# Kernel optimization log

Hardware: AMD Instinct MI355X
Metric: run time of the kernel (lower is better)

The kernel has to match this reference:

```python
import jax, jax.numpy as jnp
import numpy as np

B, DIM, IN_DIM, H, W = 4, 512, 256, 64, 64
DOWN = IN_DIM // 2          # 128
QK = DOWN // 8              # 16
EPS = 1e-5


def conv2d(x, w, b, pad=0, dil=1):
    y = jax.lax.conv_general_dilated(
        x, w, window_strides=(1, 1),
        padding=[(pad, pad), (pad, pad)],
        rhs_dilation=(dil, dil),
        dimension_numbers=('NCHW', 'OIHW', 'NCHW'))
    return y + b[None, :, None, None]


def bn(x, g, bt, m, v):
    # inference-mode BatchNorm2d with running stats
    scale = (g * jax.lax.rsqrt(v + EPS))[None, :, None, None]
    return (x - m[None, :, None, None]) * scale + bt[None, :, None, None]


def prelu(x, a):
    return jnp.where(x >= 0, x, a * x)


def setup_inputs() -> dict:
    key = jax.random.key(0)
    ks = iter(jax.random.split(key, 64))
    d = {}
    d['x'] = jax.random.normal(next(ks), (B, DIM, H, W), dtype=jnp.float32)

    def conv_params(name, cout, cin, k):
        d[name + '_w'] = jax.random.normal(next(ks), (cout, cin, k, k), jnp.float32) * 0.05
        d[name + '_b'] = jax.random.normal(next(ks), (cout,), jnp.float32) * 0.05

    def bn_params(name, c):
        d[name + '_g'] = 1.0 + 0.1 * jax.random.normal(next(ks), (c,), jnp.float32)
        d[name + '_bt'] = 0.1 * jax.random.normal(next(ks), (c,), jnp.float32)
        d[name + '_m'] = 0.1 * jax.random.normal(next(ks), (c,), jnp.float32)
        d[name + '_v'] = 0.5 + jax.random.uniform(next(ks), (c,), jnp.float32)

    def prelu_param(name):
        d[name] = jnp.full((1,), 0.25, jnp.float32)

    conv_params('dc', IN_DIM, DIM, 3);  bn_params('dc_bn', IN_DIM); prelu_param('dc_a')
    conv_params('c1', DOWN, IN_DIM, 1); bn_params('c1_bn', DOWN);   prelu_param('c1_a')
    conv_params('c2', DOWN, IN_DIM, 3); bn_params('c2_bn', DOWN);   prelu_param('c2_a')
    conv_params('q', QK, DOWN, 1)
    conv_params('k', QK, DOWN, 1)
    conv_params('v', DOWN, DOWN, 1)
    d['gamma2'] = jnp.full((1,), 0.1, jnp.float32)  # torch init is 0; nonzero to exercise the path
    conv_params('c3', DOWN, IN_DIM, 1); bn_params('c3_bn', DOWN);   prelu_param('c3_a')
    conv_params('f', IN_DIM, 3 * DOWN, 1); bn_params('f_bn', IN_DIM); prelu_param('f_a')
    return d


def reference(x,
              dc_w, dc_b, dc_bn_g, dc_bn_bt, dc_bn_m, dc_bn_v, dc_a,
              c1_w, c1_b, c1_bn_g, c1_bn_bt, c1_bn_m, c1_bn_v, c1_a,
              c2_w, c2_b, c2_bn_g, c2_bn_bt, c2_bn_m, c2_bn_v, c2_a,
              q_w, q_b, k_w, k_b, v_w, v_b, gamma2,
              c3_w, c3_b, c3_bn_g, c3_bn_bt, c3_bn_m, c3_bn_v, c3_a,
              f_w, f_b, f_bn_g, f_bn_bt, f_bn_m, f_bn_v, f_a):
    # down_conv: 3x3 conv + BN + PReLU
    x = prelu(bn(conv2d(x, dc_w, dc_b, pad=1), dc_bn_g, dc_bn_bt, dc_bn_m, dc_bn_v), dc_a)
    # branch 1: 1x1 conv
    c1 = prelu(bn(conv2d(x, c1_w, c1_b), c1_bn_g, c1_bn_bt, c1_bn_m, c1_bn_v), c1_a)
    # branch 2: dilated 3x3 conv + non-local self-attention
    c2 = prelu(bn(conv2d(x, c2_w, c2_b, pad=2, dil=2), c2_bn_g, c2_bn_bt, c2_bn_m, c2_bn_v), c2_a)
    b, c, h, w = c2.shape
    hw = h * w
    q = conv2d(c2, q_w, q_b).reshape(b, QK, hw)   # [B, C/8, HW]
    k = conv2d(c2, k_w, k_b).reshape(b, QK, hw)
    v = conv2d(c2, v_w, v_b).reshape(b, c, hw)
    energy = jnp.einsum('bcn,bcm->bnm', q, k)     # [B, HW, HW]
    attn = jax.nn.softmax(energy, axis=-1)
    out2 = jnp.einsum('bcm,bnm->bcn', v, attn).reshape(b, c, h, w)
    out2 = gamma2 * out2 + c2
    # branch 3: global avg pool -> 1x1 conv -> broadcast (bilinear upsample of 1x1 is constant)
    pooled = jnp.mean(x, axis=(2, 3), keepdims=True)  # [B, IN_DIM, 1, 1]
    c3 = prelu(bn(conv2d(pooled, c3_w, c3_b), c3_bn_g, c3_bn_bt, c3_bn_m, c3_bn_v), c3_a)
    c3 = jnp.broadcast_to(c3, (b, DOWN, h, w))
    # fuse
    cat = jnp.concatenate([c1, out2, c3], axis=1)
    return prelu(bn(conv2d(cat, f_w, f_b), f_bn_g, f_bn_bt, f_bn_m, f_bn_v), f_a)
```

## Files before the change

### kernel.cpp

```cpp
#include <hip/hip_runtime.h>
#include <hip/hip_bf16.h>
#include <math.h>

#define HW 4096
#define EPSV 1e-5f

typedef unsigned short ushort;
typedef __attribute__((ext_vector_type(8))) short bf16x8;
typedef __attribute__((ext_vector_type(4))) float f32x4;

__device__ inline ushort f2bf(float f) {
    __hip_bfloat16 h = __float2bfloat16(f);
    return *reinterpret_cast<ushort*>(&h);
}
__device__ inline float bf2f(ushort u) {
    unsigned int v = ((unsigned int)u) << 16;
    return __uint_as_float(v);
}

template<int C>
__global__ __launch_bounds__(256) void to_chlast_bf16(
    const float* __restrict__ src, ushort* __restrict__ dst)
{
    const int b = blockIdx.z, c0 = blockIdx.y * 64, p0 = blockIdx.x * 64;
    const int tid = threadIdx.x;
    __shared__ float sT[64][65];
    for (int i = tid; i < 4096; i += 256) {
        const int ch = i >> 6, px = i & 63;
        sT[ch][px] = src[(size_t)(b * C + c0 + ch) * HW + p0 + px];
    }
    __syncthreads();
    const int px = tid >> 2, seg = tid & 3;
    ushort tmp[16];
    #pragma unroll
    for (int j = 0; j < 16; ++j) tmp[j] = f2bf(sT[seg * 16 + j][px]);
    ushort* d = dst + (size_t)(b * HW + p0 + px) * C + c0 + seg * 16;
    *(uint4*)d = *(uint4*)&tmp[0];
    *(uint4*)(d + 8) = *(uint4*)&tmp[8];
}

template<int CIN, int COUT>
__global__ __launch_bounds__(256) void pack_w3x3(
    const float* __restrict__ w, ushort* __restrict__ wpk)
{
    const int idx = blockIdx.x * 256 + threadIdx.x;
    constexpr int total = 9 * (CIN / 32) * COUT * 32;
    if (idx >= total) return;
    const int ci_in = idx & 31;
    int rest = idx >> 5;
    const int co = rest % COUT; rest /= COUT;
    const int cc = rest % (CIN / 32);
    const int tap = rest / (CIN / 32);
    wpk[idx] = f2bf(w[((size_t)co * CIN + cc * 32 + ci_in) * 9 + tap]);
}

__global__ __launch_bounds__(256) void pack_w1x1(
    const float* __restrict__ w, ushort* __restrict__ o,
    int K, int stride, int total)
{
    const int idx = blockIdx.x * 256 + threadIdx.x;
    if (idx >= total) return;
    const int co = idx / K, k = idx - co * K;
    o[idx] = f2bf(w[(size_t)co * stride + k]);
}

__global__ __launch_bounds__(256) void zero_pool(float* __restrict__ p)
{
    p[blockIdx.x * 256 + threadIdx.x] = 0.f;
}

template<int CIN, int COUT, int COTILE, int DIL, int ROWS, int OMODE>
__global__ __launch_bounds__(256, OMODE == 0 ? 4 : 2) void conv3x3_fused(
    const ushort* __restrict__ xin,
    const ushort* __restrict__ wpk,
    const float* __restrict__ bias, const float* __restrict__ bng,
    const float* __restrict__ bnb, const float* __restrict__ bnm,
    const float* __restrict__ bnv, const float* __restrict__ al,
    void* __restrict__ outv,
    float* __restrict__ pool)
{
    constexpr int HR = ROWS + 2 * DIL;
    constexpr int NC = 64 + 2 * DIL;
    constexpr int MT = COTILE / 16;
    constexpr int WPR = 4 / ROWS;
    constexpr int NT = ROWS;
    constexpr int SAS = 40;
    constexpr int CH = CIN / 32;
    constexpr int NA = HR * NC * 4;
    constexpr int NREG = (NA + 255) / 256;
    constexpr int WCH = 9 * MT * 64;
    constexpr int WPT = (WCH + 255) / 256;

    const int tid = threadIdx.x;
    const int wave = tid >> 6, lane = tid & 63;
    const int l15 = lane & 15, quad = lane >> 4;
    const int b = blockIdx.z;
    const int cob = blockIdx.y;
    const int co0 = cob * COTILE;
    const int h0 = blockIdx.x * ROWS;
    const int row = wave / WPR;
    const int ntbase = (wave % WPR) * NT;

    __shared__ __align__(16) ushort sA[HR * NC * SAS];
    __shared__ __align__(16) ushort sW[WCH * 8];

    f32x4 acc[MT][NT];
    #pragma unroll
    for (int mt = 0; mt < MT; ++mt)
        #pragma unroll
        for (int nt = 0; nt < NT; ++nt) acc[mt][nt] = (f32x4){0.f, 0.f, 0.f, 0.f};

    #pragma unroll 1
    for (int cc = 0; cc < CH; ++cc) {
        if (cc != 0) __syncthreads();
        #pragma unroll
        for (int k = 0; k < NREG; ++k) {
            const int i = tid + k * 256;
            if (i < NA) {
                const int p = i >> 2, seg = i & 3;
                const int r = p / NC, c = p - r * NC;
                const int grow = h0 - DIL + r, gcol = c - DIL;
                uint4 val = {0u, 0u, 0u, 0u};
                if (grow >= 0 && grow < 64 && gcol >= 0 && gcol < 64)
                    val = *(const uint4*)&xin[((size_t)(b * 64 + grow) * 64 + gcol) * CIN
                                              + cc * 32 + seg * 8];
                *(uint4*)&sA[p * SAS + seg * 8] = val;
            }
        }
        #pragma unroll
        for (int k = 0; k < WPT; ++k) {
            const int i = tid + k * 256;
            if (i < WCH) {
                const int tap = i / (MT * 64);
                const int r = i - tap * (MT * 64);
                const int mt = r >> 6, n = r & 63;
                const uint4 wv = *(const uint4*)&wpk[
                    ((size_t)(tap * (CIN / 32) + cc) * COUT + co0 + mt * 16 + (n & 15)) * 32
                    + (n >> 4) * 8];
                *(uint4*)&sW[i * 8] = wv;
            }
        }
        __syncthreads();

        #pragma unroll
        for (int tap = 0; tap < 9; ++tap) {
            const int ty = tap / 3, tx = tap - ty * 3;
            const int rl = row + ty * DIL;
            bf16x8 wf[MT];
            #pragma unroll
            for (int mt = 0; mt < MT; ++mt)
                wf[mt] = *(const bf16x8*)&sW[((tap * MT + mt) * 64 + lane) * 8];
            #pragma unroll
            for (int nt = 0; nt < NT; ++nt) {
                const int cl = (ntbase + nt) * 16 + l15 + tx * DIL;
                const bf16x8 bp = *(const bf16x8*)&sA[(rl * NC + cl) * SAS + quad * 8];
                #pragma unroll
                for (int mt = 0; mt < MT; ++mt)
                    acc[mt][nt] = __builtin_amdgcn_mfma_f32_16x16x32_bf16(
                        wf[mt], bp, acc[mt][nt], 0, 0, 0);
            }
        }
    }

    const float a = al[0];

    if constexpr (OMODE == 0) {
        __syncthreads();
        ushort* sT = sA;
        #pragma unroll
        for (int mt = 0; mt < MT; ++mt) {
            float sc[4], sh[4], psum[4];
            #pragma unroll
            for (int rr = 0; rr < 4; ++rr) {
                const int co = co0 + mt * 16 + quad * 4 + rr;
                sc[rr] = bng[co] * rsqrtf(bnv[co] + EPSV);
                sh[rr] = (bias[co] - bnm[co]) * sc[rr] + bnb[co];
                psum[rr] = 0.f;
            }
            #pragma unroll
            for (int nt = 0; nt < NT; ++nt) {
                float tv[4];
                #pragma unroll
                for (int rr = 0; rr < 4; ++rr) {
                    float t = acc[mt][nt][rr] * sc[rr] + sh[rr];
                    t = t >= 0.f ? t : a * t;
                    tv[rr] = t;
                    psum[rr] += t;
                }
                ushort4 u;
                u.x = f2bf(tv[0]); u.y = f2bf(tv[1]);
                u.z = f2bf(tv[2]); u.w = f2bf(tv[3]);
                const int px = (ntbase + nt) * 16 + l15;
                *(ushort4*)&sT[(row * 64 + px) * 40 + mt * 16 + quad * 4] = u;
            }
            #pragma unroll
            for (int rr = 0; rr < 4; ++rr) {
                float v = psum[rr];
                v += __shfl_xor(v, 1);
                v += __shfl_xor(v, 2);
                v += __shfl_xor(v, 4);
                v += __shfl_xor(v, 8);
                if (l15 == 0)
                    atomicAdd(&pool[b * 256 + co0 + mt * 16 + quad * 4 + rr], v);
            }
        }
        __syncthreads();
        ushort* dst = (ushort*)outv;
        const int p = tid >> 1, half = tid & 1;
        const uint4 v0 = *(const uint4*)&sT[p * 40 + half * 16];
        const uint4 v1 = *(const uint4*)&sT[p * 40 + half * 16 + 8];
        const size_t off = ((size_t)(b * 4096 + (h0 + (p >> 6)) * 64 + (p & 63))) * 256
                           + co0 + half * 16;
        *(uint4*)&dst[off] = v0;
        *(uint4*)&dst[off + 8] = v1;
    } else {
        float* out = (float*)outv;
        #pragma unroll
        for (int mt = 0; mt < MT; ++mt)
            #pragma unroll
            for (int rr = 0; rr < 4; ++rr) {
                const int co = co0 + mt * 16 + quad * 4 + rr;
                const float sc = bng[co] * rsqrtf(bnv[co] + EPSV);
                const float sh = (bias[co] - bnm[co]) * sc + bnb[co];
                #pragma unroll
                for (int nt = 0; nt < NT; ++nt) {
                    float t = acc[mt][nt][rr] * sc + sh;
                    t = t >= 0.f ? t : a * t;
                    out[((size_t)(b * COUT + co) * 64 + h0 + row) * 64
                        + (ntbase + nt) * 16 + l15] = t;
                }
            }
    }
}

template<int CIN, int COUT, bool BNACT, int OMODE>
__global__ __launch_bounds__(256) void gemm1x1_cl(
    const ushort* __restrict__ xin,
    const ushort* __restrict__ wbf,
    const float* __restrict__ bias, const float* __restrict__ bng,
    const float* __restrict__ bnb, const float* __restrict__ bnm,
    const float* __restrict__ bnv, const float* __restrict__ al,
    const float* __restrict__ ebias, void* __restrict__ outv,
    int ostride, int ocol)
{
    const int tid = threadIdx.x;
    const int wave = tid >> 6, lane = tid & 63;
    const int l15 = lane & 15, quad = lane >> 4;
    const int pix0 = blockIdx.x * 128 + wave * 32;
    const int co0 = blockIdx.y * 64;

    f32x4 acc[4][2];
    #pragma unroll
    for (int mt = 0; mt < 4; ++mt)
        #pragma unroll
        for (int nt = 0; nt < 2; ++nt) acc[mt][nt] = (f32x4){0.f, 0.f, 0.f, 0.f};

    #pragma unroll 2
    for (int cc = 0; cc < CIN / 32; ++cc) {
        bf16x8 aw[4], bp[2];
        #pragma unroll
        for (int mt = 0; mt < 4; ++mt)
            aw[mt] = *(const bf16x8*)&wbf[(size_t)(co0 + mt * 16 + l15) * CIN + cc * 32 + quad * 8];
        #pragma unroll
        for (int nt = 0; nt < 2; ++nt)
            bp[nt] = *(const bf16x8*)&xin[(size_t)(pix0 + nt * 16 + l15) * CIN + cc * 32 + quad * 8];
        #pragma unroll
        for (int mt = 0; mt < 4; ++mt)
            #pragma unroll
            for (int nt = 0; nt < 2; ++nt)
                acc[mt][nt] = __builtin_amdgcn_mfma_f32_16x16x32_bf16(
                    aw[mt], bp[nt], acc[mt][nt], 0, 0, 0);
    }

    const int bI = pix0 >> 12;
    const float a = BNACT ? al[0] : 0.f;

    if (OMODE == 0) {
        float* out = (float*)outv;
        #pragma unroll
        for (int mt = 0; mt < 4; ++mt)
            #pragma unroll
            for (int r = 0; r < 4; ++r) {
                const int co = co0 + mt * 16 + quad * 4 + r;
                float bb = bias[co];
                if (ebias) bb += ebias[bI * COUT + co];
                float scale = 1.f, shift = bb;
                if (BNACT) {
                    scale = bng[co] * rsqrtf(bnv[co] + EPSV);
                    shift = bb * scale + (bnb[co] - bnm[co] * scale);
                }
                #pragma unroll
                for (int nt = 0; nt < 2; ++nt) {
                    float t = acc[mt][nt][r] * scale + shift;
                    if (BNACT) t = t >= 0.f ? t : a * t;
                    out[((size_t)(bI * COUT + co)) * HW + (pix0 & 4095) + nt * 16 + l15] = t;
                }
            }
    } else {
        __shared__ ushort sT[4][32][68];
        #pragma unroll
        for (int mt = 0; mt < 4; ++mt)
            #pragma unroll
            for (int r = 0; r < 4; ++r) {
                const int co = co0 + mt * 16 + quad * 4 + r;
                float bb = bias[co];
                float scale = 1.f, shift = bb;
                if (BNACT) {
                    scale = bng[co] * rsqrtf(bnv[co] + EPSV);
                    shift = bb * scale + (bnb[co] - bnm[co] * scale);
                }
                #pragma unroll
                for (int nt = 0; nt < 2; ++nt) {
                    float t = acc[mt][nt][r] * scale + shift;
                    if (BNACT) t = t >= 0.f ? t : a * t;
                    sT[wave][nt * 16 + l15][mt * 16 + quad * 4 + r] = f2bf(t);
                }
            }
        __syncthreads();
        const int p = lane >> 1, half = lane & 1;
        ushort* out = (ushort*)outv;
        #pragma unroll
        for (int seg = 0; seg < 4; ++seg) {
            uint2 a0 = *(uint2*)&sT[wave][p][half * 32 + seg * 8];
            uint2 a1 = *(uint2*)&sT[wave][p][half * 32 + seg * 8 + 4];
            uint4 vv = {a0.x, a0.y, a1.x, a1.y};
            *(uint4*)&out[(size_t)(pix0 + p) * ostride + ocol + co0 + half * 32 + seg * 8] = vv;
        }
    }
}

template<int CIN, bool BNACT, bool OUTBF16>
__global__ __launch_bounds__(256) void conv1x1_kernel(
    const float* __restrict__ in0,
    const float* __restrict__ wgt, int wstride, int COUT,
    const float* __restrict__ bias, const float* __restrict__ al,
    void* __restrict__ outv)
{
    const int tid = threadIdx.x;
    const int b = blockIdx.z, co0 = blockIdx.y * 64, p0 = blockIdx.x * 64;
    const int cg = tid >> 4, pg = tid & 15;
    const int c0l = cg * 4, w0 = pg * 4;

    __shared__ __align__(16) float sIn[16 * 64];
    __shared__ __align__(16) float sW[16 * 68];

    float acc[4][4] = {};

    for (int cc = 0; cc < CIN; cc += 16) {
        {
            int i = tid;
            #pragma unroll
            for (int it = 0; it < 4; ++it, i += 256) {
                const int px = i & 63, ci = i >> 6;
                sIn[ci * 64 + px] = in0[(size_t)(b * CIN + cc + ci) * HW + p0 + px];
            }
            i = tid;
            #pragma unroll
            for (int it = 0; it < 4; ++it, i += 256) {
                const int ci = i & 15, co = i >> 4;
                sW[ci * 68 + co] = wgt[(co0 + co) * wstride + cc + ci];
            }
        }
        __syncthreads();
        #pragma unroll
        for (int ci = 0; ci < 16; ++ci) {
            const float4 iv = *(const float4*)&sIn[ci * 64 + w0];
            const float4 wv = *(const float4*)&sW[ci * 68 + c0l];
            const float ia[4] = {iv.x, iv.y, iv.z, iv.w};
            const float wa[4] = {wv.x, wv.y, wv.z, wv.w};
            #pragma unroll
            for (int i2 = 0; i2 < 4; ++i2)
                #pragma unroll
                for (int j = 0; j < 4; ++j)
                    acc[i2][j] = fmaf(wa[i2], ia[j], acc[i2][j]);
        }
        __syncthreads();
    }

    const float a = BNACT ? al[0] : 0.f;
    #pragma unroll
    for (int i2 = 0; i2 < 4; ++i2) {
        const int co = co0 + c0l + i2;
        const float shift = bias[co];
        float r[4];
        #pragma unroll
        for (int j = 0; j < 4; ++j) {
            float t = acc[i2][j] + shift;
            r[j] = (BNACT && t < 0.f) ? a * t : t;
        }
        const size_t base = (size_t)(b * COUT + co) * HW + p0 + w0;
        if (OUTBF16) {
            ushort* out = (ushort*)outv;
            #pragma unroll
            for (int j = 0; j < 4; ++j) out[base + j] = f2bf(r[j]);
        } else {
            float* out = (float*)outv;
            *(float4*)&out[base] = make_float4(r[0], r[1], r[2], r[3]);
        }
    }
}

__global__ __launch_bounds__(256) void qk_kernel(
    const float* __restrict__ c2g, const float* __restrict__ qw,
    const float* __restrict__ qb2, const float* __restrict__ kw,
    const float* __restrict__ kb2, ushort* __restrict__ qpack,
    ushort* __restrict__ kpack)
{
    const int b = blockIdx.y, p0 = blockIdx.x * 64, tid = threadIdx.x;
    __shared__ float sC[128][64];
    __shared__ float sWq[16][128];
    __shared__ float sWk[16][128];
    for (int i = tid; i < 8192; i += 256) {
        const int px = i & 63, ci = i >> 6;
        sC[ci][px] = c2g[(size_t)(b * 128 + ci) * HW + p0 + px];
    }
    for (int i = tid; i < 2048; i += 256) {
        const int ci = i & 127, co = i >> 7;
        sWq[co][ci] = qw[co * 128 + ci];
        sWk[co][ci] = kw[co * 128 + ci];
    }
    __syncthreads();
    const int px = tid & 63, grp = tid >> 6;
    const int co0 = (grp & 1) * 8;
    const bool isK = grp >= 2;
    const float* sWp = isK ? &sWk[0][0] : &sWq[0][0];
    float acc[8] = {};
    for (int ci = 0; ci < 128; ++ci) {
        const float xv = sC[ci][px];
        #pragma unroll
        for (int j = 0; j < 8; ++j)
            acc[j] = fmaf(sWp[(co0 + j) * 128 + ci], xv, acc[j]);
    }
    const float* bsrc = isK ? kb2 : qb2;
    ushort* osrc = isK ? kpack : qpack;
    const size_t base = (size_t)(b * 4096 + p0 + px) * 32;
    #pragma unroll
    for (int j = 0; j < 8; ++j) {
        osrc[base + co0 + j] = f2bf(acc[j] + bsrc[co0 + j]);
        osrc[base + 16 + co0 + j] = 0;
    }
}

__global__ __launch_bounds__(256) void attn_flash(
    const ushort* __restrict__ qpack,
    const ushort* __restrict__ kpack,
    const ushort* __restrict__ vpackT,
    ushort* __restrict__ opart,
    float* __restrict__ Mpart,
    float* __restrict__ Spart)
{
    const int tid = threadIdx.x;
    const int wave = tid >> 6, lane = tid & 63;
    const int l15 = lane & 15, quad = lane >> 4;
    const int b = blockIdx.z, j = blockIdx.y;
    const int n0w = blockIdx.x * 128 + wave * 32;
    const int m_begin = j * 512;

    __shared__ __align__(16) ushort sV[2][128][40];
    __shared__ __align__(16) ushort sP[4][2][16][40];

    const bf16x8 bq0 = *(const bf16x8*)(qpack + ((size_t)(b * 4096 + n0w + l15) * 32 + quad * 8));
    const bf16x8 bq1 = *(const bf16x8*)(qpack + ((size_t)(b * 4096 + n0w + 16 + l15) * 32 + quad * 8));
    const f32x4 z = {0.f, 0.f, 0.f, 0.f};

    float runM0 = -3e30f, runM1 = -3e30f;
    #pragma unroll 2
    for (int t = 0; t < 8; ++t) {
        const int m0 = m_begin + t * 64;
        #pragma unroll
        for (int ms = 0; ms < 4; ++ms) {
            const bf16x8 ak = *(const bf16x8*)(
                kpack + ((size_t)(b * 4096 + m0 + ms * 16 + l15) * 32 + quad * 8));
            const f32x4 s0 = __builtin_amdgcn_mfma_f32_16x16x32_bf16(ak, bq0, z, 0, 0, 0);
            const f32x4 s1 = __builtin_amdgcn_mfma_f32_16x16x32_bf16(ak, bq1, z, 0, 0, 0);
            runM0 = fmaxf(runM0, fmaxf(fmaxf(s0[0], s0[1]), fmaxf(s0[2], s0[3])));
            runM1 = fmaxf(runM1, fmaxf(fmaxf(s1[0], s1[1]), fmaxf(s1[2], s1[3])));
        }
    }
    runM0 = fmaxf(runM0, __shfl_xor(runM0, 16));
    runM0 = fmaxf(runM0, __shfl_xor(runM0, 32));
    runM1 = fmaxf(runM1, __shfl_xor(runM1, 16));
    runM1 = fmaxf(runM1, __shfl_xor(runM1, 32));
    const float Ms0 = runM0 * 1.44269504f;
    const float Ms1 = runM1 * 1.44269504f;

    float runS0 = 0.f, runS1 = 0.f;
    f32x4 oacc0[8], oacc1[8];
    #pragma unroll
    for (int cs = 0; cs < 8; ++cs) {
        oacc0[cs] = (f32x4){0.f, 0.f, 0.f, 0.f};
        oacc1[cs] = (f32x4){0.f, 0.f, 0.f, 0.f};
    }

    const int stc = tid >> 1, stseg = tid & 1;

    {
        uint4 v0 = *(const uint4*)&vpackT[(size_t)(b * 128 + stc) * HW + m_begin + stseg * 16];
        uint4 v1 = *(const uint4*)&vpackT[(size_t)(b * 128 + stc) * HW + m_begin + stseg * 16 + 8];
        *(uint4*)&sV[0][stc][stseg * 16] = v0;
        *(uint4*)&sV[0][stc][stseg * 16 + 8] = v1;
    }
    __syncthreads();

    #pragma unroll 1
    for (int t = 0; t < 16; ++t) {
        const int m0 = m_begin + t * 32;
        const int buf = t & 1;
        uint4 nv0, nv1;
        const bool more = (t + 1 < 16);
        if (more) {
            const size_t nb = (size_t)(b * 128 + stc) * HW + m0 + 32 + stseg * 16;
            nv0 = *(const uint4*)&vpackT[nb];
            nv1 = *(const uint4*)&vpackT[nb + 8];
        }
        f32x4 s0[2], s1[2];
        #pragma unroll
        for (int ms = 0; ms < 2; ++ms) {
            const bf16x8 ak = *(const bf16x8*)(
                kpack + ((size_t)(b * 4096 + m0 + ms * 16 + l15) * 32 + quad * 8));
            s0[ms] = __builtin_amdgcn_mfma_f32_16x16x32_bf16(ak, bq0, z, 0, 0, 0);
            s1[ms] = __builtin_amdgcn_mfma_f32_16x16x32_bf16(ak, bq1, z, 0, 0, 0);
        }
        #pragma unroll
        for (int ms = 0; ms < 2; ++ms) {
            float p0[4], p1[4];
            #pragma unroll
            for (int r = 0; r < 4; ++r) {
                p0[r] = __builtin_amdgcn_exp2f(fmaf(s0[ms][r], 1.44269504f, -Ms0));
                p1[r] = __builtin_amdgcn_exp2f(fmaf(s1[ms][r], 1.44269504f, -Ms1));
                runS0 += p0[r];
                runS1 += p1[r];
            }
            ushort4 u0, u1;
            u0.x = f2bf(p0[0]); u0.y = f2bf(p0[1]); u0.z = f2bf(p0[2]); u0.w = f2bf(p0[3]);
            u1.x = f2bf(p1[0]); u1.y = f2bf(p1[1]); u1.z = f2bf(p1[2]); u1.w = f2bf(p1[3]);
            *(uint2*)&sP[wave][0][l15][ms * 16 + quad * 4] = *(uint2*)&u0;
            *(uint2*)&sP[wave][1][l15][ms * 16 + quad * 4] = *(uint2*)&u1;
        }
        asm volatile("s_waitcnt lgkmcnt(0)" ::: "memory");
        const bf16x8 ap0 = *(const bf16x8*)&sP[wave][0][l15][quad * 8];
        const bf16x8 ap1 = *(const bf16x8*)&sP[wave][1][l15][quad * 8];
        #pragma unroll
        for (int cs = 0; cs < 8; ++cs) {
            const bf16x8 bv = *(const bf16x8*)&sV[buf][cs * 16 + l15][quad * 8];
            oacc0[cs] = __builtin_amdgcn_mfma_f32_16x16x32_bf16(ap0, bv, oacc0[cs], 0, 0, 0);
            oacc1[cs] = __builtin_amdgcn_mfma_f32_16x16x32_bf16(ap1, bv, oacc1[cs], 0, 0, 0);
        }
        if (more) {
            *(uint4*)&sV[buf ^ 1][stc][stseg * 16] = nv0;
            *(uint4*)&sV[buf ^ 1][stc][stseg * 16 + 8] = nv1;
            __syncthreads();
        }
    }

    runS0 += __shfl_xor(runS0, 16);
    runS0 += __shfl_xor(runS0, 32);
    runS1 += __shfl_xor(runS1, 16);
    runS1 += __shfl_xor(runS1, 32);
    if (lane < 32) {
        const float Mv = (lane < 16) ? runM0 : runM1;
        const float Sv = (lane < 16) ? runS0 : runS1;
        const int n = n0w + ((lane < 16) ? 0 : 16) + l15;
        Mpart[((size_t)b * 8 + j) * 4096 + n] = Mv;
        Spart[((size_t)b * 8 + j) * 4096 + n] = Sv;
    }
    #pragma unroll
    for (int cs = 0; cs < 8; ++cs)
        #pragma unroll
        for (int r = 0; r < 4; ++r) {
            const int n = n0w + quad * 4 + r;
            opart[(((size_t)b * 8 + j) * 4096 + n) * 128 + cs * 16 + l15] = f2bf(oacc0[cs][r]);
            opart[(((size_t)b * 8 + j) * 4096 + n + 16) * 128 + cs * 16 + l15] = f2bf(oacc1[cs][r]);
        }
}

__global__ __launch_bounds__(256) void attn_combine(
    const ushort* __restrict__ opart, const float* __restrict__ Mpart,
    const float* __restrict__ Spart, const float* __restrict__ c2g,
    const float* __restrict__ gamma2, ushort* __restrict__ catb)
{
    const int b = blockIdx.y, n0 = blockIdx.x * 32, tid = threadIdx.x;
    __shared__ float sC2[128][33];
    __shared__ float sWj[8][32];
    if (tid < 32) {
        const int n = n0 + tid;
        float Mj[8], Sj[8];
        #pragma unroll
        for (int j = 0; j < 8; ++j) {
            Mj[j] = Mpart[((size_t)b * 8 + j) * 4096 + n];
            Sj[j] = Spart[((size_t)b * 8 + j) * 4096 + n];
        }
        float M = -3e30f;
        #pragma unroll
        for (int j = 0; j < 8; ++j) M = fmaxf(M, Mj[j]);
        float St = 0.f, e[8];
        #pragma unroll
        for (int j = 0; j < 8; ++j) { e[j] = __expf(Mj[j] - M); St += Sj[j] * e[j]; }
        const float inv = 1.0f / St;
        #pragma unroll
        for (int j = 0; j < 8; ++j) sWj[j][tid] = e[j] * inv;
    }
    #pragma unroll
    for (int e = 0; e < 16; ++e) {
        const int idx = tid + e * 256;
        const int c = idx >> 5, n = idx & 31;
        sC2[c][n] = c2g[(size_t)(b * 128 + c) * HW + n0 + n];
    }
    __syncthreads();
    const float g2 = gamma2[0];
    #pragma unroll
    for (int e = 0; e < 16; ++e) {
        const int idx = tid + e * 256;
        const int n = idx >> 7, c = idx & 127;
        float s = 0.f;
        #pragma unroll
        for (int j = 0; j < 8; ++j)
            s += bf2f(opart[(((size_t)b * 8 + j) * 4096 + n0 + n) * 128 + c]) * sWj[j][n];
        catb[(size_t)(b * 4096 + n0 + n) * 256 + 128 + c] = f2bf(fmaf(g2, s, sC2[c][n]));
    }
}

__global__ __launch_bounds__(256) void c3_fbias_kernel(
    const float* __restrict__ pool, const float* __restrict__ c3w,
    const float* __restrict__ c3b, const float* __restrict__ bng,
    const float* __restrict__ bnb, const float* __restrict__ bnm,
    const float* __restrict__ bnv, const float* __restrict__ al,
    const float* __restrict__ fw, float* __restrict__ fbias)
{
    const int b = blockIdx.x, tid = threadIdx.x;
    __shared__ float sp[256];
    __shared__ float sc3[128];
    sp[tid] = pool[b * 256 + tid] * (1.0f / 4096.0f);
    __syncthreads();
    if (tid < 128) {
        float acc = c3b[tid];
        for (int ci = 0; ci < 256; ++ci) acc = fmaf(c3w[tid * 256 + ci], sp[ci], acc);
        const float scale = bng[tid] * rsqrtf(bnv[tid] + EPSV);
        float t = (acc - bnm[tid]) * scale + bnb[tid];
        const float a = al[0];
        sc3[tid] = t >= 0.f ? t : a * t;
    }
    __syncthreads();
    float f = 0.f;
    for (int j = 0; j < 128; ++j) f = fmaf(fw[tid * 384 + 256 + j], sc3[j], f);
    fbias[b * 256 + tid] = f;
}

extern "C" void kernel_launch(void* const* d_in, const int* in_sizes, int n_in,
                              void* d_out, int out_size, void* d_ws, size_t ws_size,
                              hipStream_t stream)
{
    const float* x     = (const float*)d_in[0];
    const float* dc_w  = (const float*)d_in[1];
    const float* dc_b  = (const float*)d_in[2];
    const float* dc_g  = (const float*)d_in[3];
    const float* dc_bt = (const float*)d_in[4];
    const float* dc_m  = (const float*)d_in[5];
    const float* dc_v  = (const float*)d_in[6];
    const float* dc_a  = (const float*)d_in[7];
    const float* c1_w  = (const float*)d_in[8];
    const float* c1_b  = (const float*)d_in[9];
    const float* c1_g  = (const float*)d_in[10];
    const float* c1_bt = (const float*)d_in[11];
    const float* c1_m  = (const float*)d_in[12];
    const float* c1_v  = (const float*)d_in[13];
    const float* c1_a  = (const float*)d_in[14];
    const float* c2_w  = (const float*)d_in[15];
    const float* c2_b  = (const float*)d_in[16];
    const float* c2_g  = (const float*)d_in[17];
    const float* c2_bt = (const float*)d_in[18];
    const float* c2_m  = (const float*)d_in[19];
    const float* c2_v  = (const float*)d_in[20];
    const float* c2_a  = (const float*)d_in[21];
    const float* q_w   = (const float*)d_in[22];
    const float* q_b   = (const float*)d_in[23];
    const float* k_w   = (const float*)d_in[24];
    const float* k_b   = (const float*)d_in[25];
    const float* v_w   = (const float*)d_in[26];
    const float* v_b   = (const float*)d_in[27];
    const float* gamma2= (const float*)d_in[28];
    const float* c3_w  = (const float*)d_in[29];
    const float* c3_b  = (const float*)d_in[30];
    const float* c3_g  = (const float*)d_in[31];
    const float* c3_bt = (const float*)d_in[32];
    const float* c3_m  = (const float*)d_in[33];
    const float* c3_v  = (const float*)d_in[34];
    const float* c3_a  = (const float*)d_in[35];
    const float* f_w   = (const float*)d_in[36];
    const float* f_b   = (const float*)d_in[37];
    const float* f_g   = (const float*)d_in[38];
    const float* f_bt  = (const float*)d_in[39];
    const float* f_m   = (const float*)d_in[40];
    const float* f_v   = (const float*)d_in[41];
    const float* f_a   = (const float*)d_in[42];

    char* base = (char*)d_ws;
    ushort* xbf   = (ushort*)base;
    ushort* opart = (ushort*)base;
    ushort* qpk   = (ushort*)(base + 33554432);
    ushort* kpk   = (ushort*)(base + 34603008);
    ushort* vbh   = (ushort*)(base + 35651584);
    float*  c2b   = (float*)(base + 39845888);
    ushort* xpbf  = (ushort*)(base + 50331648);
    ushort* catb  = (ushort*)(base + 58720256);
    ushort* wdcp  = (ushort*)(base + 75497472);
    ushort* wc2p  = (ushort*)(base + 77856768);
    ushort* wc1b  = (ushort*)(base + 78446592);
    ushort* wfb   = (ushort*)(base + 78512128);
    float*  poolb = (float*)(base + 78643200);
    float*  fbb   = (float*)(base + 78647296);
    float*  Mpart = (float*)(base + 78651392);
    float*  Spart = (float*)(base + 79175680);

    pack_w3x3<512, 256><<<dim3((9*16*256*32 + 255)/256), 256, 0, stream>>>(dc_w, wdcp);
    pack_w3x3<256, 128><<<dim3((9*8*128*32 + 255)/256), 256, 0, stream>>>(c2_w, wc2p);
    pack_w1x1<<<dim3((32768 + 255)/256), 256, 0, stream>>>(c1_w, wc1b, 256, 256, 32768);
    pack_w1x1<<<dim3((65536 + 255)/256), 256, 0, stream>>>(f_w, wfb, 256, 384, 65536);
    to_chlast_bf16<512><<<dim3(64, 8, 4), 256, 0, stream>>>(x, xbf);
    zero_pool<<<dim3(4), 256, 0, stream>>>(poolb);
    conv3x3_fused<512, 256, 32, 1, 2, 0><<<dim3(32, 8, 4), 256, 0, stream>>>(
        xbf, wdcp, dc_b, dc_g, dc_bt, dc_m, dc_v, dc_a, xpbf, poolb);
    c3_fbias_kernel<<<dim3(4), 256, 0, stream>>>(
        poolb, c3_w, c3_b, c3_g, c3_bt, c3_m, c3_v, c3_a, f_w, fbb);
    gemm1x1_cl<256, 128, true, 1><<<dim3(128, 2), 256, 0, stream>>>(
        xpbf, wc1b, c1_b, c1_g, c1_bt, c1_m, c1_v, c1_a, nullptr, catb, 256, 0);
    conv3x3_fused<256, 128, 32, 2, 2, 1><<<dim3(32, 4, 4), 256, 0, stream>>>(
        xpbf, wc2p, c2_b, c2_g, c2_bt, c2_m, c2_v, c2_a, c2b, nullptr);
    qk_kernel<<<dim3(64, 4), 256, 0, stream>>>(c2b, q_w, q_b, k_w, k_b, qpk, kpk);
    conv1x1_kernel<128, false, true><<<dim3(64, 2, 4), 256, 0, stream>>>(
        c2b, v_w, 128, 128, v_b, nullptr, vbh);
    attn_flash<<<dim3(32, 8, 4), 256, 0, stream>>>(qpk, kpk, vbh, opart, Mpart, Spart);
    attn_combine<<<dim3(128, 4), 256, 0, stream>>>(opart, Mpart, Spart, c2b, gamma2, catb);
    gemm1x1_cl<256, 256, true, 0><<<dim3(128, 4), 256, 0, stream>>>(
        catb, wfb, f_b, f_g, f_bt, f_m, f_v, f_a, fbb, (float*)d_out, 0, 0);
}
```

Measured before the change: 408.8 us.

## Replace two-pass attention max with online softmax using lazy rescaling

The attention kernel no longer runs a separate pass over all keys to find the row maximum. Instead it keeps a running max and rescales the sum and output accumulators only when a tile's max exceeds the running max by a threshold. This halves the QK^T MFMA and K-load work in that kernel, at the cost of per-tile cross-lane reductions and a wave-wide vote. Separately, the conv kernel now issues all global loads into registers before writing them to LDS, so more loads are in flight at once.

```diff
diff --git a/kernel.cpp b/kernel.cpp
--- a/kernel.cpp
+++ b/kernel.cpp
@@ -113,31 +113,44 @@
     #pragma unroll 1
     for (int cc = 0; cc < CH; ++cc) {
         if (cc != 0) __syncthreads();
-        #pragma unroll
-        for (int k = 0; k < NREG; ++k) {
-            const int i = tid + k * 256;
-            if (i < NA) {
-                const int p = i >> 2, seg = i & 3;
-                const int r = p / NC, c = p - r * NC;
-                const int grow = h0 - DIL + r, gcol = c - DIL;
+        {
+            uint4 xr[NREG];
+            #pragma unroll
+            for (int k = 0; k < NREG; ++k) {
+                const int i = tid + k * 256;
                 uint4 val = {0u, 0u, 0u, 0u};
-                if (grow >= 0 && grow < 64 && gcol >= 0 && gcol < 64)
-                    val = *(const uint4*)&xin[((size_t)(b * 64 + grow) * 64 + gcol) * CIN
-                                              + cc * 32 + seg * 8];
-                *(uint4*)&sA[p * SAS + seg * 8] = val;
-            }
-        }
-        #pragma unroll
-        for (int k = 0; k < WPT; ++k) {
-            const int i = tid + k * 256;
-            if (i < WCH) {
-                const int tap = i / (MT * 64);
-                const int r = i - tap * (MT * 64);
-                const int mt = r >> 6, n = r & 63;
-                const uint4 wv = *(const uint4*)&wpk[
-                    ((size_t)(tap * (CIN / 32) + cc) * COUT + co0 + mt * 16 + (n & 15)) * 32
-                    + (n >> 4) * 8];
-                *(uint4*)&sW[i * 8] = wv;
+                if (i < NA) {
+                    const int p = i >> 2, seg = i & 3;
+                    const int r = p / NC, c = p - r * NC;
+                    const int grow = h0 - DIL + r, gcol = c - DIL;
+                    if (grow >= 0 && grow < 64 && gcol >= 0 && gcol < 64)
+                        val = *(const uint4*)&xin[((size_t)(b * 64 + grow) * 64 + gcol) * CIN
+                                                  + cc * 32 + seg * 8];
+                }
+                xr[k] = val;
+            }
+            uint4 wr_[WPT];
+            #pragma unroll
+            for (int k = 0; k < WPT; ++k) {
+                const int i = tid + k * 256;
+                if (i < WCH) {
+                    const int tap = i / (MT * 64);
+                    const int r = i - tap * (MT * 64);
+                    const int mt = r >> 6, n = r & 63;
+                    wr_[k] = *(const uint4*)&wpk[
+                        ((size_t)(tap * (CIN / 32) + cc) * COUT + co0 + mt * 16 + (n & 15)) * 32
+                        + (n >> 4) * 8];
+                }
+            }
+            #pragma unroll
+            for (int k = 0; k < NREG; ++k) {
+                const int i = tid + k * 256;
+                if (i < NA) *(uint4*)&sA[(i >> 2) * SAS + (i & 3) * 8] = xr[k];
+            }
+            #pragma unroll
+            for (int k = 0; k < WPT; ++k) {
+                const int i = tid + k * 256;
+                if (i < WCH) *(uint4*)&sW[i * 8] = wr_[k];
             }
         }
         __syncthreads();
@@ -464,26 +477,6 @@
     const f32x4 z = {0.f, 0.f, 0.f, 0.f};
 
     float runM0 = -3e30f, runM1 = -3e30f;
-    #pragma unroll 2
-    for (int t = 0; t < 8; ++t) {
-        const int m0 = m_begin + t * 64;
-        #pragma unroll
-        for (int ms = 0; ms < 4; ++ms) {
-            const bf16x8 ak = *(const bf16x8*)(
-                kpack + ((size_t)(b * 4096 + m0 + ms * 16 + l15) * 32 + quad * 8));
-            const f32x4 s0 = __builtin_amdgcn_mfma_f32_16x16x32_bf16(ak, bq0, z, 0, 0, 0);
-            const f32x4 s1 = __builtin_amdgcn_mfma_f32_16x16x32_bf16(ak, bq1, z, 0, 0, 0);
-            runM0 = fmaxf(runM0, fmaxf(fmaxf(s0[0], s0[1]), fmaxf(s0[2], s0[3])));
-            runM1 = fmaxf(runM1, fmaxf(fmaxf(s1[0], s1[1]), fmaxf(s1[2], s1[3])));
-        }
-    }
-    runM0 = fmaxf(runM0, __shfl_xor(runM0, 16));
-    runM0 = fmaxf(runM0, __shfl_xor(runM0, 32));
-    runM1 = fmaxf(runM1, __shfl_xor(runM1, 16));
-    runM1 = fmaxf(runM1, __shfl_xor(runM1, 32));
-    const float Ms0 = runM0 * 1.44269504f;
-    const float Ms1 = runM1 * 1.44269504f;
-
     float runS0 = 0.f, runS1 = 0.f;
     f32x4 oacc0[8], oacc1[8];
     #pragma unroll
@@ -521,6 +514,46 @@
             s0[ms] = __builtin_amdgcn_mfma_f32_16x16x32_bf16(ak, bq0, z, 0, 0, 0);
             s1[ms] = __builtin_amdgcn_mfma_f32_16x16x32_bf16(ak, bq1, z, 0, 0, 0);
         }
+
+        float tM0 = fmaxf(fmaxf(fmaxf(s0[0][0], s0[0][1]), fmaxf(s0[0][2], s0[0][3])),
+                          fmaxf(fmaxf(s0[1][0], s0[1][1]), fmaxf(s0[1][2], s0[1][3])));
+        float tM1 = fmaxf(fmaxf(fmaxf(s1[0][0], s1[0][1]), fmaxf(s1[0][2], s1[0][3])),
+                          fmaxf(fmaxf(s1[1][0], s1[1][1]), fmaxf(s1[1][2], s1[1][3])));
+        tM0 = fmaxf(tM0, __shfl_xor(tM0, 16));
+        tM0 = fmaxf(tM0, __shfl_xor(tM0, 32));
+        tM1 = fmaxf(tM1, __shfl_xor(tM1, 16));
+        tM1 = fmaxf(tM1, __shfl_xor(tM1, 32));
+        if (__any(tM0 > runM0 + 8.f)) {
+            const float nM = fmaxf(runM0, tM0);
+            const float sc = __builtin_amdgcn_exp2f((runM0 - nM) * 1.44269504f);
+            runS0 *= sc;
+            float scr[4];
+            #pragma unroll
+            for (int r = 0; r < 4; ++r) scr[r] = __shfl(sc, quad * 4 + r);
+            #pragma unroll
+            for (int cs = 0; cs < 8; ++cs) {
+                oacc0[cs][0] *= scr[0]; oacc0[cs][1] *= scr[1];
+                oacc0[cs][2] *= scr[2]; oacc0[cs][3] *= scr[3];
+            }
+            runM0 = nM;
+        }
+        if (__any(tM1 > runM1 + 8.f)) {
+            const float nM = fmaxf(runM1, tM1);
+            const float sc = __builtin_amdgcn_exp2f((runM1 - nM) * 1.44269504f);
+            runS1 *= sc;
+            float scr[4];
+            #pragma unroll
+            for (int r = 0; r < 4; ++r) scr[r] = __shfl(sc, quad * 4 + r);
+            #pragma unroll
+            for (int cs = 0; cs < 8; ++cs) {
+                oacc1[cs][0] *= scr[0]; oacc1[cs][1] *= scr[1];
+                oacc1[cs][2] *= scr[2]; oacc1[cs][3] *= scr[3];
+            }
+            runM1 = nM;
+        }
+        const float Ms0 = runM0 * 1.44269504f;
+        const float Ms1 = runM1 * 1.44269504f;
+
         #pragma unroll
         for (int ms = 0; ms < 2; ++ms) {
             float p0[4], p1[4];
```

Result: slower. 461.8 us (+13.0%).
